# Kernel tuning notes

Hardware: AMD Instinct MI355X
Metric: run time of the kernel (lower is better)

The kernel has to match this reference:

```python
import jax, jax.numpy as jnp
import numpy as np

LOG_2PI = np.float32(np.log(2.0 * np.pi))


def _expect(features, labels, pi, mu, sigma):
    # features [N,A], labels [N], pi [C,K], mu [C,K,A], sigma [C,K,A,A]
    d = features.shape[1]
    K = pi.shape[1]
    pi_n = pi[labels]                      # [N,K]
    mu_n = mu[labels]                      # [N,K,A]
    # invert / slogdet per (class, cluster) once, then gather (same math as
    # inverting the per-sample gathered sigma, but C*K inversions not N*K)
    inv_sigma = jnp.linalg.inv(sigma)[labels]          # [N,K,A,A]
    logdet = jnp.linalg.slogdet(sigma)[1][labels]      # [N,K]
    diff = features[:, None, :] - mu_n                 # [N,K,A]
    dist = jnp.einsum('nkd,nkde,nke->nk', diff, inv_sigma, diff)
    # NOTE: sign of the d*log(2pi) term follows the original code verbatim
    log_p = -(dist - d * LOG_2PI + logdet) / 2.0       # [N,K]
    onehot = jax.nn.one_hot(jnp.argmax(log_p, axis=1), K, dtype=features.dtype)
    q_un = onehot * pi_n
    return q_un / (q_un.sum(axis=1, keepdims=True) + 1e-30)


def setup_inputs() -> dict:
    key = jax.random.key(0)
    ks = jax.random.split(key, 6)
    N, C, K, A = 2048, 100, 4, 128
    features = jax.random.normal(ks[0], (N, A), dtype=jnp.float32)
    weight = jax.random.normal(ks[1], (C, A), dtype=jnp.float32) * 0.05
    bias = jnp.zeros((C,), dtype=jnp.float32)
    pi = jax.random.uniform(ks[2], (C, K), dtype=jnp.float32) + 0.1
    pi = pi / pi.sum(axis=1, keepdims=True)
    mu = jax.random.normal(ks[3], (C, K, A), dtype=jnp.float32)
    # SPD covariance stack: B B^T / A + I
    B = jax.random.normal(ks[4], (C, K, A, A), dtype=jnp.float32) * 0.3
    sigma = jnp.einsum('ckij,cklj->ckil', B, B) / A + jnp.eye(A, dtype=jnp.float32)
    labels = jax.random.randint(ks[5], (N,), 0, C, dtype=jnp.int64)
    ratio = jnp.float32(0.5)
    return {"features": features, "weight": weight, "bias": bias,
            "pi": pi, "mu": mu, "sigma": sigma, "labels": labels,
            "ratio": ratio}


def reference(features, weight, bias, pi, mu, sigma, labels, ratio):
    N, A = features.shape
    C, K = pi.shape
    y = features @ weight.T + bias                     # fc(features)  [N,C]
    # NxW_ij - NxW_kj : row j of W minus row label[n] of W, per sample
    diff_w = weight[None, :, :] - weight[labels][:, None, :]   # [N,C,A]
    q = _expect(features, labels, pi, mu, sigma)               # [N,K]
    onehot_q = jax.nn.one_hot(jnp.argmax(q, axis=1), K, dtype=features.dtype)
    CV = jnp.einsum('nkde,nk->nde', sigma[labels], onehot_q)   # [N,A,A]
    # diagonal of ratio * (dW) CV (dW)^T, computed without the [N,C,C] matrix
    sigma2 = ratio * jnp.einsum('nca,nab,ncb->nc', diff_w, CV, diff_w)
    aug = y + 0.5 * sigma2                                     # [N,C]
    logp = jax.nn.log_softmax(aug, axis=-1)
    loss = -jnp.mean(jnp.take_along_axis(logp, labels[:, None], axis=1))
    return (loss, y)
```

## Files before the change

kernel.cpp:

```cpp
#include <hip/hip_runtime.h>
#include <hip/hip_bf16.h>
#include <cmath>

#define N_S    2048
#define C_CLS  100
#define K_CL   4
#define A_DIM  128
#define LDSROW 132
#define NB     16
#define MAXPER 96

__global__ __launch_bounds__(256) void k_bucket(
    const int* __restrict__ labels, int* __restrict__ cntg, int* __restrict__ idxg)
{
    __shared__ int cntL[C_CLS];
    const int t = threadIdx.x;
    if (t < C_CLS) cntL[t] = 0;
    __syncthreads();
    for (int n = t; n < N_S; n += 256) {
        int c = labels[n];
        int slot = atomicAdd(&cntL[c], 1);
        if (slot < MAXPER) idxg[c * MAXPER + slot] = n;
    }
    __syncthreads();
    if (t < C_CLS) cntg[t] = min(cntL[t], MAXPER);
}

__device__ __forceinline__ float gj_invert_lds(
    float* As, float* Rbuf, float* DinvS, int tid)
{
    const int lane = tid & 63;
    const int wv   = tid >> 6;
    float logdet = 0.0f;

    for (int t = 0; t < 8; ++t) {
        const int p0 = NB * t;

        if (wv == 0) {
            const int r = lane >> 2, cg = lane & 3;
            float4 dv = *(const float4*)&As[(p0 + r) * LDSROW + p0 + 4 * cg];
            #pragma unroll
            for (int p = 0; p < NB; ++p) {
                const int sel = p & 3, pr4 = p >> 2;
                float te = (sel == 0) ? dv.x : (sel == 1) ? dv.y : (sel == 2) ? dv.z : dv.w;
                float piv = __shfl(te, (p << 2) | pr4, 64);
                float ip  = 1.0f / piv;
                logdet += __logf(piv);
                const int rowsrc = (p << 2) | cg;
                float4 prs;
                prs.x = __shfl(dv.x, rowsrc, 64) * ip;
                prs.y = __shfl(dv.y, rowsrc, 64) * ip;
                prs.z = __shfl(dv.z, rowsrc, 64) * ip;
                prs.w = __shfl(dv.w, rowsrc, 64) * ip;
                if (cg == pr4) (&prs.x)[sel] = ip;
                float f = __shfl(te, (lane & ~3) | pr4, 64);
                if (r == p) {
                    dv = prs;
                } else {
                    dv.x -= f * prs.x; dv.y -= f * prs.y;
                    dv.z -= f * prs.z; dv.w -= f * prs.w;
                    if (cg == pr4) (&dv.x)[sel] = -f * ip;
                }
            }
            DinvS[r * 17 + 4 * cg + 0] = dv.x;
            DinvS[r * 17 + 4 * cg + 1] = dv.y;
            DinvS[r * 17 + 4 * cg + 2] = dv.z;
            DinvS[r * 17 + 4 * cg + 3] = dv.w;
        }
        __syncthreads();

        {
            const int rr = tid >> 5, j4c = tid & 31;
            float4 o;
            if ((j4c >> 2) == t) {
                const int cg = j4c & 3;
                o.x = DinvS[rr * 17 + 4 * cg + 0];
                o.y = DinvS[rr * 17 + 4 * cg + 1];
                o.z = DinvS[rr * 17 + 4 * cg + 2];
                o.w = DinvS[rr * 17 + 4 * cg + 3];
            } else {
                o.x = 0.f; o.y = 0.f; o.z = 0.f; o.w = 0.f;
                #pragma unroll 4
                for (int k = 0; k < NB; ++k) {
                    const float a = DinvS[rr * 17 + k];
                    const float4 s4 = *(const float4*)&As[(p0 + k) * LDSROW + 4 * j4c];
                    o.x += a * s4.x; o.y += a * s4.y; o.z += a * s4.z; o.w += a * s4.w;
                }
            }
            *(float4*)&Rbuf[rr * A_DIM + 4 * j4c] = o;
        }
        __syncthreads();

        if (tid < 448) {
            const int rgi = tid >> 4;
            const int cp  = tid & 15;
            const int rga = (rgi < 4 * t) ? rgi : rgi + 4;
            const int row0 = 4 * rga;
            const int c0 = 8 * cp, c1 = 8 * cp + 4;
            const bool pcol = ((cp >> 1) == t);
            float4 a00, a01, a10, a11, a20, a21, a30, a31;
            if (pcol) {
                a00 = a01 = a10 = a11 = a20 = a21 = a30 = a31 = (float4){0, 0, 0, 0};
            } else {
                a00 = *(const float4*)&As[(row0 + 0) * LDSROW + c0];
                a01 = *(const float4*)&As[(row0 + 0) * LDSROW + c1];
                a10 = *(const float4*)&As[(row0 + 1) * LDSROW + c0];
                a11 = *(const float4*)&As[(row0 + 1) * LDSROW + c1];
                a20 = *(const float4*)&As[(row0 + 2) * LDSROW + c0];
                a21 = *(const float4*)&As[(row0 + 2) * LDSROW + c1];
                a30 = *(const float4*)&As[(row0 + 3) * LDSROW + c0];
                a31 = *(const float4*)&As[(row0 + 3) * LDSROW + c1];
            }
            #pragma unroll 4
            for (int k = 0; k < NB; ++k) {
                const float4 r0 = *(const float4*)&Rbuf[k * A_DIM + c0];
                const float4 r1 = *(const float4*)&Rbuf[k * A_DIM + c1];
                const float f0 = As[(row0 + 0) * LDSROW + p0 + k];
                const float f1 = As[(row0 + 1) * LDSROW + p0 + k];
                const float f2 = As[(row0 + 2) * LDSROW + p0 + k];
                const float f3 = As[(row0 + 3) * LDSROW + p0 + k];
                a00.x -= f0 * r0.x; a00.y -= f0 * r0.y; a00.z -= f0 * r0.z; a00.w -= f0 * r0.w;
                a01.x -= f0 * r1.x; a01.y -= f0 * r1.y; a01.z -= f0 * r1.z; a01.w -= f0 * r1.w;
                a10.x -= f1 * r0.x; a10.y -= f1 * r0.y; a10.z -= f1 * r0.z; a10.w -= f1 * r0.w;
                a11.x -= f1 * r1.x; a11.y -= f1 * r1.y; a11.z -= f1 * r1.z; a11.w -= f1 * r1.w;
                a20.x -= f2 * r0.x; a20.y -= f2 * r0.y; a20.z -= f2 * r0.z; a20.w -= f2 * r0.w;
                a21.x -= f2 * r1.x; a21.y -= f2 * r1.y; a21.z -= f2 * r1.z; a21.w -= f2 * r1.w;
                a30.x -= f3 * r0.x; a30.y -= f3 * r0.y; a30.z -= f3 * r0.z; a30.w -= f3 * r0.w;
                a31.x -= f3 * r1.x; a31.y -= f3 * r1.y; a31.z -= f3 * r1.z; a31.w -= f3 * r1.w;
            }
            *(float4*)&As[(row0 + 0) * LDSROW + c0] = a00;
            *(float4*)&As[(row0 + 0) * LDSROW + c1] = a01;
            *(float4*)&As[(row0 + 1) * LDSROW + c0] = a10;
            *(float4*)&As[(row0 + 1) * LDSROW + c1] = a11;
            *(float4*)&As[(row0 + 2) * LDSROW + c0] = a20;
            *(float4*)&As[(row0 + 2) * LDSROW + c1] = a21;
            *(float4*)&As[(row0 + 3) * LDSROW + c0] = a30;
            *(float4*)&As[(row0 + 3) * LDSROW + c1] = a31;
        }
        {
            const int rr = tid >> 5, j4c = tid & 31;
            *(float4*)&As[(p0 + rr) * LDSROW + 4 * j4c] =
                *(const float4*)&Rbuf[rr * A_DIM + 4 * j4c];
        }
        __syncthreads();
    }
    return logdet;
}

__global__ __launch_bounds__(512, 2) void k_invert_score(
    const float* __restrict__ sigma, const float* __restrict__ mu,
    const float* __restrict__ features, const int* __restrict__ cntg,
    const int* __restrict__ idxg, float* __restrict__ score)
{
    __shared__ __align__(16) float As[A_DIM * LDSROW];
    __shared__ __align__(16) float Scratch[NB * A_DIM + 16*33];
    __shared__ float DinvS[NB * 17];
    __shared__ float ldS;

    const int tid = threadIdx.x;
    const int bid = blockIdx.x;
    const int cl  = bid >> 2;

    const float4* src = (const float4*)(sigma + (size_t)bid * A_DIM * A_DIM);
    for (int e4 = tid; e4 < A_DIM * 32; e4 += 512) {
        int i = e4 >> 5, j4 = e4 & 31;
        *(float4*)&As[i * LDSROW + 4 * j4] = src[e4];
    }
    __syncthreads();

    float logdet = gj_invert_lds(As, Scratch, DinvS, tid);
    if (tid == 0) ldS = logdet;
    __syncthreads();
    const float ld = ldS;

    float* Dbuf = Scratch;
    float* Par  = Scratch + NB * A_DIM;
    const int s16 = tid >> 5;
    const int fc  = tid & 31;
    const int cnt = cntg[cl];
    const float4 muv = ((const float4*)mu)[bid * 32 + fc];

    for (int c0 = 0; c0 < cnt; c0 += 16) {
        const int m = cnt - c0 < 16 ? cnt - c0 : 16;
        if (s16 < m) {
            const int n = idxg[cl * MAXPER + c0 + s16];
            const float4 f = ((const float4*)features)[n * 32 + fc];
            float4 dv;
            dv.x = f.x - muv.x; dv.y = f.y - muv.y;
            dv.z = f.z - muv.z; dv.w = f.w - muv.w;
            *(float4*)&Dbuf[s16 * A_DIM + 4 * fc] = dv;
        }
        __syncthreads();
        if (s16 < m) {
            float4 p = {0.f, 0.f, 0.f, 0.f};
            #pragma unroll 4
            for (int i = 0; i < A_DIM; ++i) {
                const float  d = Dbuf[s16 * A_DIM + i];
                const float4 a = *(const float4*)&As[i * LDSROW + 4 * fc];
                p.x += d * a.x; p.y += d * a.y; p.z += d * a.z; p.w += d * a.w;
            }
            const float4 dj = *(const float4*)&Dbuf[s16 * A_DIM + 4 * fc];
            Par[s16 * 33 + fc] = p.x * dj.x + p.y * dj.y + p.z * dj.z + p.w * dj.w;
        }
        __syncthreads();
        if (tid < m) {
            const int n = idxg[cl * MAXPER + c0 + tid];
            float q = 0.f;
            #pragma unroll
            for (int j = 0; j < 32; ++j) q += Par[tid * 33 + j];
            score[n * K_CL + (bid & 3)] = q + ld;
        }
        __syncthreads();
    }
}

__global__ __launch_bounds__(256) void k_gprep(
    const float* __restrict__ sigma, const float* __restrict__ weight,
    float* __restrict__ gdiag, float* __restrict__ gcol)
{
    __shared__ __align__(16) float Ss[A_DIM * A_DIM];
    __shared__ __align__(16) float Ws[C_CLS * A_DIM];
    const int tid = threadIdx.x, bid = blockIdx.x;
    const int cl  = bid >> 2;
    const int lane = tid & 63, wv = tid >> 6;

    const float4* src = (const float4*)(sigma + (size_t)bid * A_DIM * A_DIM);
    for (int e4 = tid; e4 < A_DIM * 32; e4 += 256)
        ((float4*)Ss)[e4] = src[e4];
    const float4* wsrc = (const float4*)weight;
    for (int e4 = tid; e4 < C_CLS * 32; e4 += 256)
        ((float4*)Ws)[e4] = wsrc[e4];
    __syncthreads();

    const float wc0 = Ws[cl * A_DIM + lane];
    const float wc1 = Ws[cl * A_DIM + 64 + lane];
    const int cbeg = wv * 25;

    for (int g = 0; g < 5; ++g) {
        const int c0 = cbeg + g * 5;
        const float* w0 = &Ws[(c0 + 0) * A_DIM];
        const float* w1 = &Ws[(c0 + 1) * A_DIM];
        const float* w2 = &Ws[(c0 + 2) * A_DIM];
        const float* w3 = &Ws[(c0 + 3) * A_DIM];
        const float* w4 = &Ws[(c0 + 4) * A_DIM];
        float h00 = 0.f, h01 = 0.f, h02 = 0.f, h03 = 0.f, h04 = 0.f;
        float h10 = 0.f, h11 = 0.f, h12 = 0.f, h13 = 0.f, h14 = 0.f;
        #pragma unroll 4
        for (int i = 0; i < A_DIM; ++i) {
            const float s0 = Ss[i * A_DIM + lane];
            const float s1 = Ss[i * A_DIM + 64 + lane];
            const float b0 = w0[i], b1 = w1[i], b2 = w2[i], b3 = w3[i], b4 = w4[i];
            h00 += b0 * s0; h10 += b0 * s1;
            h01 += b1 * s0; h11 += b1 * s1;
            h02 += b2 * s0; h12 += b2 * s1;
            h03 += b3 * s0; h13 += b3 * s1;
            h04 += b4 * s0; h14 += b4 * s1;
        }
        #define GOUT(HA, HB, CC)                                            \
        {                                                                   \
            const int c = c0 + (CC);                                        \
            float pd = (HA) * Ws[c * A_DIM + lane]                          \
                     + (HB) * Ws[c * A_DIM + 64 + lane];                    \
            float pc = (HA) * wc0 + (HB) * wc1;                             \
            _Pragma("unroll")                                               \
            for (int off = 32; off; off >>= 1) {                            \
                pd += __shfl_xor(pd, off, 64);                              \
                pc += __shfl_xor(pc, off, 64);                              \
            }                                                               \
            if (lane == 0) {                                                \
                gdiag[bid * C_CLS + c] = pd;                                \
                gcol [bid * C_CLS + c] = pc;                                \
            }                                                               \
        }
        GOUT(h00, h10, 0)
        GOUT(h01, h11, 1)
        GOUT(h02, h12, 2)
        GOUT(h03, h13, 3)
        GOUT(h04, h14, 4)
        #undef GOUT
    }
}

__global__ __launch_bounds__(128) void k_out(
    const float* __restrict__ features, const float* __restrict__ weight,
    const float* __restrict__ bias, const int* __restrict__ labels,
    const float* __restrict__ score, const float* __restrict__ gdiag,
    const float* __restrict__ gcol, const float* __restrict__ ratio_p,
    float* __restrict__ y, float* __restrict__ loss)
{
    __shared__ __align__(16) float xs[A_DIM];
    __shared__ float red[2], red2[2], acl_s;
    const int n = blockIdx.x, t = threadIdx.x;
    xs[t] = features[(size_t)n * A_DIM + t];
    __syncthreads();

    const int cl = labels[n];
    const float ratio = *ratio_p;

    float s0 = score[n * 4 + 0], s1 = score[n * 4 + 1];
    float s2 = score[n * 4 + 2], s3 = score[n * 4 + 3];
    int ks = 0; float bs = s0;
    if (s1 < bs) { bs = s1; ks = 1; }
    if (s2 < bs) { bs = s2; ks = 2; }
    if (s3 < bs) { bs = s3; ks = 3; }

    const int base = (cl * 4 + ks) * C_CLS;
    const float gll = gdiag[base + cl];
    float aug = -INFINITY;
    if (t < C_CLS) {
        const float4* wr = (const float4*)(weight + t * A_DIM);
        const float4* xr = (const float4*)xs;
        float acc = bias[t];
        #pragma unroll
        for (int j = 0; j < 32; ++j) {
            float4 a = xr[j], b = wr[j];
            acc += a.x * b.x + a.y * b.y + a.z * b.z + a.w * b.w;
        }
        y[(size_t)n * C_CLS + t] = acc;
        aug = acc + 0.5f * ratio * (gdiag[base + t] - 2.0f * gcol[base + t] + gll);
    }

    float m = aug;
    #pragma unroll
    for (int off = 32; off; off >>= 1) m = fmaxf(m, __shfl_xor(m, off, 64));
    if ((t & 63) == 0) red[t >> 6] = m;
    __syncthreads();
    m = fmaxf(red[0], red[1]);

    float e = (t < C_CLS) ? expf(aug - m) : 0.0f;
    #pragma unroll
    for (int off = 32; off; off >>= 1) e += __shfl_xor(e, off, 64);
    if ((t & 63) == 0) red2[t >> 6] = e;
    if (t == cl) acl_s = aug;
    __syncthreads();

    if (t == 0) {
        float sum = red2[0] + red2[1];
        float lp = acl_s - m - logf(sum);
        atomicAdd(loss, -lp * (1.0f / (float)N_S));
    }
}

extern "C" void kernel_launch(void* const* d_in, const int* in_sizes, int n_in,
                              void* d_out, int out_size, void* d_ws, size_t ws_size,
                              hipStream_t stream) {
    const float* features = (const float*)d_in[0];
    const float* weight   = (const float*)d_in[1];
    const float* bias     = (const float*)d_in[2];
    const float* mu       = (const float*)d_in[4];
    const float* sigma    = (const float*)d_in[5];
    const int*   labels   = (const int*)d_in[6];
    const float* ratio    = (const float*)d_in[7];

    float* out   = (float*)d_out;
    float* yout  = out + 1;
    float* score = (float*)d_ws;
    float* gdiag = score + N_S * K_CL;
    float* gcol  = gdiag + C_CLS * K_CL * C_CLS;
    int*   cntg  = (int*)(gcol + C_CLS * K_CL * C_CLS);
    int*   idxg  = cntg + C_CLS;

    hipMemsetAsync(d_out, 0, sizeof(float), stream);

    k_bucket      <<<dim3(1),            dim3(256), 0, stream>>>(labels, cntg, idxg);
    k_invert_score<<<dim3(C_CLS * K_CL), dim3(512), 0, stream>>>(sigma, mu, features,
                                                                 cntg, idxg, score);
    k_gprep       <<<dim3(C_CLS * K_CL), dim3(256), 0, stream>>>(sigma, weight, gdiag, gcol);
    k_out         <<<dim3(N_S),          dim3(128), 0, stream>>>(features, weight, bias, labels,
                                                                 score, gdiag, gcol, ratio, yout, out);
}
```

Measured before the change: 253.1 us.

## Drop weight LDS staging in gprep and batch samples per block in output kernel

k_gprep stops copying the whole weight matrix into shared memory. It reads weight rows through uniform global (scalar) loads in templated sweeps of 10/10/5 classes, which cuts LDS use so two blocks can fit per CU. k_out now stages a transposed, padded copy of weight in LDS once per block and processes 8 samples per 256-thread block, two at a time. Per-sample loss is accumulated in a shared atomic before one global atomic. Costs include extra register pressure from 10-wide accumulators and more per-block setup and barriers in k_out.

Result: faster. 218.5 us (-13.7%).

```diff
diff --git a/kernel.cpp b/kernel.cpp
--- a/kernel.cpp
+++ b/kernel.cpp
@@ -9,6 +9,8 @@
 #define LDSROW 132
 #define NB     16
 #define MAXPER 96
+#define WTPAD  101
+#define SPB    8
 
 __global__ __launch_bounds__(256) void k_bucket(
     const int* __restrict__ labels, int* __restrict__ cntg, int* __restrict__ idxg)
@@ -214,12 +216,50 @@
     }
 }
 
-__global__ __launch_bounds__(256) void k_gprep(
+template<int R>
+__device__ __forceinline__ void gsweep(
+    const float* __restrict__ Ss, const float* __restrict__ weight,
+    int c0, int lane, float wc0, float wc1, int bid,
+    float* __restrict__ gdiag, float* __restrict__ gcol)
+{
+    const int c0u = __builtin_amdgcn_readfirstlane(c0);
+    const float* __restrict__ wr = weight + (size_t)c0u * A_DIM;
+    float h0[R], h1[R];
+    #pragma unroll
+    for (int r = 0; r < R; ++r) { h0[r] = 0.f; h1[r] = 0.f; }
+    #pragma unroll 2
+    for (int i = 0; i < A_DIM; ++i) {
+        const float s0 = Ss[i * A_DIM + lane];
+        const float s1 = Ss[i * A_DIM + 64 + lane];
+        #pragma unroll
+        for (int r = 0; r < R; ++r) {
+            const float b = wr[r * A_DIM + i];
+            h0[r] += b * s0; h1[r] += b * s1;
+        }
+    }
+    #pragma unroll
+    for (int r = 0; r < R; ++r) {
+        const int c = c0 + r;
+        float pd = h0[r] * weight[c * A_DIM + lane]
+                 + h1[r] * weight[c * A_DIM + 64 + lane];
+        float pc = h0[r] * wc0 + h1[r] * wc1;
+        #pragma unroll
+        for (int off = 32; off; off >>= 1) {
+            pd += __shfl_xor(pd, off, 64);
+            pc += __shfl_xor(pc, off, 64);
+        }
+        if (lane == 0) {
+            gdiag[bid * C_CLS + c] = pd;
+            gcol [bid * C_CLS + c] = pc;
+        }
+    }
+}
+
+__global__ __launch_bounds__(256, 2) void k_gprep(
     const float* __restrict__ sigma, const float* __restrict__ weight,
     float* __restrict__ gdiag, float* __restrict__ gcol)
 {
     __shared__ __align__(16) float Ss[A_DIM * A_DIM];
-    __shared__ __align__(16) float Ws[C_CLS * A_DIM];
     const int tid = threadIdx.x, bid = blockIdx.x;
     const int cl  = bid >> 2;
     const int lane = tid & 63, wv = tid >> 6;
@@ -227,118 +267,93 @@
     const float4* src = (const float4*)(sigma + (size_t)bid * A_DIM * A_DIM);
     for (int e4 = tid; e4 < A_DIM * 32; e4 += 256)
         ((float4*)Ss)[e4] = src[e4];
-    const float4* wsrc = (const float4*)weight;
-    for (int e4 = tid; e4 < C_CLS * 32; e4 += 256)
-        ((float4*)Ws)[e4] = wsrc[e4];
-    __syncthreads();
-
-    const float wc0 = Ws[cl * A_DIM + lane];
-    const float wc1 = Ws[cl * A_DIM + 64 + lane];
+    __syncthreads();
+
+    const float wc0 = weight[cl * A_DIM + lane];
+    const float wc1 = weight[cl * A_DIM + 64 + lane];
     const int cbeg = wv * 25;
 
-    for (int g = 0; g < 5; ++g) {
-        const int c0 = cbeg + g * 5;
-        const float* w0 = &Ws[(c0 + 0) * A_DIM];
-        const float* w1 = &Ws[(c0 + 1) * A_DIM];
-        const float* w2 = &Ws[(c0 + 2) * A_DIM];
-        const float* w3 = &Ws[(c0 + 3) * A_DIM];
-        const float* w4 = &Ws[(c0 + 4) * A_DIM];
-        float h00 = 0.f, h01 = 0.f, h02 = 0.f, h03 = 0.f, h04 = 0.f;
-        float h10 = 0.f, h11 = 0.f, h12 = 0.f, h13 = 0.f, h14 = 0.f;
-        #pragma unroll 4
-        for (int i = 0; i < A_DIM; ++i) {
-            const float s0 = Ss[i * A_DIM + lane];
-            const float s1 = Ss[i * A_DIM + 64 + lane];
-            const float b0 = w0[i], b1 = w1[i], b2 = w2[i], b3 = w3[i], b4 = w4[i];
-            h00 += b0 * s0; h10 += b0 * s1;
-            h01 += b1 * s0; h11 += b1 * s1;
-            h02 += b2 * s0; h12 += b2 * s1;
-            h03 += b3 * s0; h13 += b3 * s1;
-            h04 += b4 * s0; h14 += b4 * s1;
-        }
-        #define GOUT(HA, HB, CC)                                            \
-        {                                                                   \
-            const int c = c0 + (CC);                                        \
-            float pd = (HA) * Ws[c * A_DIM + lane]                          \
-                     + (HB) * Ws[c * A_DIM + 64 + lane];                    \
-            float pc = (HA) * wc0 + (HB) * wc1;                             \
-            _Pragma("unroll")                                               \
-            for (int off = 32; off; off >>= 1) {                            \
-                pd += __shfl_xor(pd, off, 64);                              \
-                pc += __shfl_xor(pc, off, 64);                              \
-            }                                                               \
-            if (lane == 0) {                                                \
-                gdiag[bid * C_CLS + c] = pd;                                \
-                gcol [bid * C_CLS + c] = pc;                                \
-            }                                                               \
-        }
-        GOUT(h00, h10, 0)
-        GOUT(h01, h11, 1)
-        GOUT(h02, h12, 2)
-        GOUT(h03, h13, 3)
-        GOUT(h04, h14, 4)
-        #undef GOUT
-    }
-}
-
-__global__ __launch_bounds__(128) void k_out(
+    gsweep<10>(Ss, weight, cbeg,      lane, wc0, wc1, bid, gdiag, gcol);
+    gsweep<10>(Ss, weight, cbeg + 10, lane, wc0, wc1, bid, gdiag, gcol);
+    gsweep<5> (Ss, weight, cbeg + 20, lane, wc0, wc1, bid, gdiag, gcol);
+}
+
+__global__ __launch_bounds__(256) void k_out(
     const float* __restrict__ features, const float* __restrict__ weight,
     const float* __restrict__ bias, const int* __restrict__ labels,
     const float* __restrict__ score, const float* __restrict__ gdiag,
     const float* __restrict__ gcol, const float* __restrict__ ratio_p,
     float* __restrict__ y, float* __restrict__ loss)
 {
-    __shared__ __align__(16) float xs[A_DIM];
-    __shared__ float red[2], red2[2], acl_s;
-    const int n = blockIdx.x, t = threadIdx.x;
-    xs[t] = features[(size_t)n * A_DIM + t];
-    __syncthreads();
-
-    const int cl = labels[n];
+    __shared__ float Wt[A_DIM * WTPAD];
+    __shared__ float bs[C_CLS];
+    __shared__ __align__(16) float xs[2][A_DIM];
+    __shared__ float red[2][2], red2[2][2], acl_s[2], lsum;
+
+    const int tid  = threadIdx.x;
+    const int half = tid >> 7;
+    const int t    = tid & 127;
+
+    for (int u = tid; u < C_CLS * 32; u += 256) {
+        const int c = u >> 5, j4 = u & 31;
+        const float4 w = ((const float4*)weight)[u];
+        Wt[(4 * j4 + 0) * WTPAD + c] = w.x;
+        Wt[(4 * j4 + 1) * WTPAD + c] = w.y;
+        Wt[(4 * j4 + 2) * WTPAD + c] = w.z;
+        Wt[(4 * j4 + 3) * WTPAD + c] = w.w;
+    }
+    if (tid < C_CLS) bs[tid] = bias[tid];
+    if (tid == 0) lsum = 0.f;
+    __syncthreads();
+
     const float ratio = *ratio_p;
 
-    float s0 = score[n * 4 + 0], s1 = score[n * 4 + 1];
-    float s2 = score[n * 4 + 2], s3 = score[n * 4 + 3];
-    int ks = 0; float bs = s0;
-    if (s1 < bs) { bs = s1; ks = 1; }
-    if (s2 < bs) { bs = s2; ks = 2; }
-    if (s3 < bs) { bs = s3; ks = 3; }
-
-    const int base = (cl * 4 + ks) * C_CLS;
-    const float gll = gdiag[base + cl];
-    float aug = -INFINITY;
-    if (t < C_CLS) {
-        const float4* wr = (const float4*)(weight + t * A_DIM);
-        const float4* xr = (const float4*)xs;
-        float acc = bias[t];
+    for (int p = 0; p < SPB; p += 2) {
+        const int n = blockIdx.x * SPB + p + half;
+        if (t < 32) ((float4*)xs[half])[t] = ((const float4*)features)[n * 32 + t];
+        __syncthreads();
+
+        const int cl = labels[n];
+        float s0 = score[n * 4 + 0], s1 = score[n * 4 + 1];
+        float s2 = score[n * 4 + 2], s3 = score[n * 4 + 3];
+        int ks = 0; float bsv = s0;
+        if (s1 < bsv) { bsv = s1; ks = 1; }
+        if (s2 < bsv) { bsv = s2; ks = 2; }
+        if (s3 < bsv) { bsv = s3; ks = 3; }
+
+        const int base = (cl * 4 + ks) * C_CLS;
+        const float gll = gdiag[base + cl];
+        float aug = -INFINITY;
+        if (t < C_CLS) {
+            float acc = bs[t];
+            #pragma unroll 4
+            for (int j = 0; j < A_DIM; ++j)
+                acc += xs[half][j] * Wt[j * WTPAD + t];
+            y[(size_t)n * C_CLS + t] = acc;
+            aug = acc + 0.5f * ratio * (gdiag[base + t] - 2.0f * gcol[base + t] + gll);
+        }
+
+        float m = aug;
         #pragma unroll
-        for (int j = 0; j < 32; ++j) {
-            float4 a = xr[j], b = wr[j];
-            acc += a.x * b.x + a.y * b.y + a.z * b.z + a.w * b.w;
-        }
-        y[(size_t)n * C_CLS + t] = acc;
-        aug = acc + 0.5f * ratio * (gdiag[base + t] - 2.0f * gcol[base + t] + gll);
-    }
-
-    float m = aug;
-    #pragma unroll
-    for (int off = 32; off; off >>= 1) m = fmaxf(m, __shfl_xor(m, off, 64));
-    if ((t & 63) == 0) red[t >> 6] = m;
-    __syncthreads();
-    m = fmaxf(red[0], red[1]);
-
-    float e = (t < C_CLS) ? expf(aug - m) : 0.0f;
-    #pragma unroll
-    for (int off = 32; off; off >>= 1) e += __shfl_xor(e, off, 64);
-    if ((t & 63) == 0) red2[t >> 6] = e;
-    if (t == cl) acl_s = aug;
-    __syncthreads();
-
-    if (t == 0) {
-        float sum = red2[0] + red2[1];
-        float lp = acl_s - m - logf(sum);
-        atomicAdd(loss, -lp * (1.0f / (float)N_S));
-    }
+        for (int off = 32; off; off >>= 1) m = fmaxf(m, __shfl_xor(m, off, 64));
+        if ((t & 63) == 0) red[half][t >> 6] = m;
+        __syncthreads();
+        m = fmaxf(red[half][0], red[half][1]);
+
+        float e = (t < C_CLS) ? expf(aug - m) : 0.0f;
+        #pragma unroll
+        for (int off = 32; off; off >>= 1) e += __shfl_xor(e, off, 64);
+        if ((t & 63) == 0) red2[half][t >> 6] = e;
+        if (t == cl) acl_s[half] = aug;
+        __syncthreads();
+
+        if (t == 0) {
+            float lp = acl_s[half] - m - logf(red2[half][0] + red2[half][1]);
+            atomicAdd(&lsum, -lp);
+        }
+        __syncthreads();
+    }
+    if (tid == 0) atomicAdd(loss, lsum * (1.0f / (float)N_S));
 }
 
 extern "C" void kernel_launch(void* const* d_in, const int* in_sizes, int n_in,
@@ -366,6 +381,6 @@
     k_invert_score<<<dim3(C_CLS * K_CL), dim3(512), 0, stream>>>(sigma, mu, features,
                                                                  cntg, idxg, score);
     k_gprep       <<<dim3(C_CLS * K_CL), dim3(256), 0, stream>>>(sigma, weight, gdiag, gcol);
-    k_out         <<<dim3(N_S),          dim3(128), 0, stream>>>(features, weight, bias, labels,
+    k_out         <<<dim3(N_S / SPB),    dim3(256), 0, stream>>>(features, weight, bias, labels,
                                                                  score, gdiag, gcol, ratio, yout, out);
 }
```
